# Kernel tuning notes

Hardware: AMD Instinct MI355X
Metric: run time of the kernel (lower is better)

The kernel has to match this reference:

```python
import jax, jax.numpy as jnp
from jax import lax
import numpy as np

B, C, H, W = 8, 192, 56, 56
N = H * W
K_CLUSTERS = 16   # num_centroids
K_NBRS = 9        # kNN neighbors
FACTOR = 2
COUT = C * FACTOR # hidden channels of graph conv
CPE_K = 7         # depthwise CPE kernel (odd)


def setup_inputs() -> dict:
    key = jax.random.key(0)
    ks = jax.random.split(key, 12)
    s = 0.02
    return {
        "x": jax.random.normal(ks[0], (B, C, H, W), jnp.float32),
        "labels": jax.random.randint(ks[1], (B, N), 0, K_CLUSTERS, jnp.int32),
        "cpe_w": jax.random.normal(ks[2], (C, 1, CPE_K, CPE_K), jnp.float32) * s,
        "cpe_b": jnp.zeros((C,), jnp.float32),
        "fc1_w": jax.random.normal(ks[3], (C, C), jnp.float32) * s,
        "fc1_b": jnp.zeros((C,), jnp.float32),
        "nn_v_w": jax.random.normal(ks[4], (2 * C, COUT), jnp.float32) * s,
        "nn_v_b": jnp.zeros((COUT,), jnp.float32),
        "nn_c_w": jax.random.normal(ks[5], (2 * C, COUT), jnp.float32) * s,
        "nn_c_b": jnp.zeros((COUT,), jnp.float32),
        "fc2_w": jax.random.normal(ks[6], (COUT, C), jnp.float32) * s,
        "fc2_b": jnp.zeros((C,), jnp.float32),
    }


def reference(x, labels, cpe_w, cpe_b, fc1_w, fc1_b, nn_v_w, nn_v_b,
              nn_c_w, nn_c_b, fc2_w, fc2_b):
    Bx, Cx, Hx, Wx = x.shape
    n = Hx * Wx
    shortcut = x
    # --- Conditional Position Encoding: depthwise conv + residual ---
    pe = lax.conv_general_dilated(
        x, cpe_w, (1, 1), "SAME", feature_group_count=Cx,
        dimension_numbers=("NCHW", "OIHW", "NCHW"))
    x = pe + cpe_b[None, :, None, None] + x
    # --- fc1: 1x1 conv ---
    xf = jnp.einsum("bchw,cd->bdhw", x, fc1_w) + fc1_b[None, :, None, None]
    xn = xf.reshape(Bx, Cx, n).transpose(0, 2, 1)  # [B,N,C]
    # --- organize_and_map: stable sort nodes by cluster label ---
    order = jnp.argsort(labels, axis=1)            # sorted pos -> orig idx (stable)
    mapping = jnp.argsort(order, axis=1)           # orig idx -> sorted pos
    xs = jnp.take_along_axis(xn, order[:, :, None], axis=1)  # [B,N,C]
    ls = jnp.take_along_axis(labels, order, axis=1)          # [B,N]
    # --- kNN on l2-normalized feats, restricted to same cluster ---
    xe = xs / jnp.maximum(jnp.linalg.norm(xs, axis=-1, keepdims=True), 1e-12)
    sq = jnp.sum(xe * xe, axis=-1)                 # [B,N]
    d2 = sq[:, :, None] + sq[:, None, :] - 2.0 * jnp.einsum("bnc,bmc->bnm", xe, xe)
    same = ls[:, :, None] == ls[:, None, :]        # [B,N,N] cluster mask
    d2 = jnp.where(same, d2, jnp.inf)
    _, nbr = lax.top_k(-d2, K_NBRS)                # [B,N,k] nearest in-cluster
    valid = jnp.take_along_axis(same, nbr, axis=2) # False when cluster < k
    # --- vertex edge conv: max_j MLP([x_i, x_j - x_i]) ---
    xj = jax.vmap(lambda xb, nb: xb[nb])(xs, nbr)  # [B,N,k,C]
    xi = xs[:, :, None, :]
    msg = jnp.concatenate([jnp.broadcast_to(xi, xj.shape), xj - xi], axis=-1)
    h = jax.nn.gelu(msg @ nn_v_w + nn_v_b)         # [B,N,k,COUT]
    h = jnp.where(valid[..., None], h, -jnp.inf)   # self is always valid
    hv = jnp.max(h, axis=2)                        # [B,N,COUT]
    # --- centroid edge conv over cluster centers (fully connected per image) ---
    onehot = (ls[:, :, None] == jnp.arange(K_CLUSTERS)[None, None, :]).astype(xs.dtype)
    cnt = jnp.maximum(onehot.sum(axis=1), 1.0)     # [B,K]
    cen = jnp.einsum("bnk,bnc->bkc", onehot, xs) / cnt[:, :, None]
    ci = cen[:, :, None, :]
    cj = cen[:, None, :, :]
    cmsg = jnp.concatenate(
        [jnp.broadcast_to(ci, (Bx, K_CLUSTERS, K_CLUSTERS, Cx)), cj - ci], axis=-1)
    hc = jnp.max(jax.nn.gelu(cmsg @ nn_c_w + nn_c_b), axis=2)  # [B,K,COUT]
    hcn = jax.vmap(lambda hb, lb: hb[lb])(hc, ls)  # scatter center feat to nodes
    hn = hv + hcn                                  # [B,N,COUT]
    # --- unshuffle back to original raster order ---
    out_nodes = jnp.take_along_axis(hn, mapping[:, :, None], axis=1)
    # --- fc2: 1x1 conv back to C, residual ---
    y = out_nodes @ fc2_w + fc2_b                  # [B,N,C]
    y = y.transpose(0, 2, 1).reshape(Bx, Cx, Hx, Wx)
    return y + shortcut
```

## Files before the change

kernel.cpp:

```cpp
#include <hip/hip_runtime.h>
#include <math.h>

#define NB 8
#define NC 192
#define NH 56
#define NW 56
#define NN 3136
#define NK 16
#define KNB 9
#define NCOUT 384
#define LPMAX 320
#define DSTRIDE 320
#define DSLOT (320 * 320)

#define FLT_INF __builtin_inff()

typedef short s16x8 __attribute__((ext_vector_type(8)));
typedef _Float16 f16x8 __attribute__((ext_vector_type(8)));
typedef float f32x4 __attribute__((ext_vector_type(4)));
typedef unsigned short us8 __attribute__((ext_vector_type(8)));
typedef unsigned short us4 __attribute__((ext_vector_type(4)));

__device__ __forceinline__ float gelu_t(float x) {
    const float k0 = 0.7978845608028654f;
    float u = k0 * (x + 0.044715f * x * x * x);
    float t = tanhf(u);
    return 0.5f * x * (1.0f + t);
}

__device__ __forceinline__ unsigned short f2bf(float f) {
    unsigned u = __float_as_uint(f);
    u += 0x7fff + ((u >> 16) & 1);
    return (unsigned short)(u >> 16);
}

__device__ __forceinline__ float bf2f(unsigned short h) {
    return __uint_as_float(((unsigned)h) << 16);
}

__global__ void order_kernel(const int* __restrict__ labels, int* __restrict__ order,
                             int* __restrict__ mapping, int* __restrict__ lsv,
                             int* __restrict__ cntk, int* __restrict__ offk) {
    int b = blockIdx.x >> 4;
    int k = blockIdx.x & 15;
    int lane = threadIdx.x;
    const int* lb = labels + (size_t)b * NN;
    int cntLess = 0, cntEq = 0;
    for (int n0 = 0; n0 < NN; n0 += 64) {
        int lab = lb[n0 + lane] & 15;
        cntLess += __popcll(__ballot(lab < k));
        cntEq += __popcll(__ballot(lab == k));
    }
    int base = cntLess;
    int run = 0;
    for (int n0 = 0; n0 < NN; n0 += 64) {
        int n = n0 + lane;
        int lab = lb[n] & 15;
        bool p = (lab == k);
        unsigned long long mask = __ballot(p);
        int rank = __popcll(mask & ((1ull << lane) - 1ull));
        if (p) {
            int pos = base + run + rank;
            order[b * NN + pos] = n;
            mapping[b * NN + n] = pos;
            lsv[b * NN + pos] = k;
        }
        run += __popcll(mask);
    }
    if (lane == 0) {
        offk[b * NK + k] = base;
        cntk[b * NK + k] = cntEq;
    }
}

__global__ __launch_bounds__(256) void conv_kernel(const float* __restrict__ X,
                                                   const float* __restrict__ W7,
                                                   const float* __restrict__ bias,
                                                   unsigned short* __restrict__ xpe) {
    __shared__ float tile[62 * 62];
    __shared__ float wl[49];
    int bc = blockIdx.x;
    int c = bc % NC;
    const float* Xp = X + (size_t)bc * NN;
    int tid = threadIdx.x;
    if (tid < 49) wl[tid] = W7[(size_t)c * 49 + tid];
    for (int idx = tid; idx < 62 * 62; idx += 256) {
        int ty = idx / 62, tx = idx % 62;
        int gy = ty - 3, gx = tx - 3;
        float v = 0.0f;
        if (gy >= 0 && gy < NH && gx >= 0 && gx < NW) v = Xp[gy * NW + gx];
        tile[idx] = v;
    }
    __syncthreads();
    float cb = bias[c];
    for (int g = tid; g < (NN / 4); g += 256) {
        int y = g / (NW / 4), x0 = (g % (NW / 4)) * 4;
        float a0 = 0.f, a1 = 0.f, a2 = 0.f, a3 = 0.f;
#pragma unroll
        for (int dy = 0; dy < 7; ++dy) {
            const float* tr = &tile[(y + dy) * 62 + x0];
#pragma unroll
            for (int dx = 0; dx < 7; ++dx) {
                float wv = wl[dy * 7 + dx];
                a0 += tr[dx] * wv;
                a1 += tr[dx + 1] * wv;
                a2 += tr[dx + 2] * wv;
                a3 += tr[dx + 3] * wv;
            }
        }
        const float* rr = &tile[(y + 3) * 62 + x0 + 3];
        us4 o;
        o[0] = f2bf(a0 + cb + rr[0]);
        o[1] = f2bf(a1 + cb + rr[1]);
        o[2] = f2bf(a2 + cb + rr[2]);
        o[3] = f2bf(a3 + cb + rr[3]);
        *(us4*)(xpe + (size_t)bc * NN + y * NW + x0) = o;
    }
}

__global__ void wcvt_all_kernel(const float* __restrict__ Wf1, const float* __restrict__ Wv,
                                const float* __restrict__ Wf2, unsigned short* __restrict__ wf1,
                                unsigned short* __restrict__ wfpmq,
                                unsigned short* __restrict__ wfq,
                                unsigned short* __restrict__ wf2) {
    int z = blockIdx.z, nt = blockIdx.x, kc = blockIdx.y;
    const float* W;
    unsigned short* Bf;
    int ldw, rowoff, KC, NT;
    bool diff = false;
    if (z == 0) { W = Wf1; Bf = wf1; ldw = NC; rowoff = 0; KC = 6; NT = 3; }
    else if (z == 1) { W = Wv; Bf = wfpmq; ldw = NCOUT; rowoff = 0; KC = 6; NT = 6; diff = true; }
    else if (z == 2) { W = Wv; Bf = wfq; ldw = NCOUT; rowoff = NC; KC = 6; NT = 6; }
    else { W = Wf2; Bf = wf2; ldw = NC; rowoff = 0; KC = 12; NT = 3; }
    if (nt >= NT || kc >= KC) return;
    int tid = threadIdx.x;
    int c = tid >> 6, l = tid & 63;
    int n = l & 15, q = l >> 4;
    int col = nt * 64 + c * 16 + n;
    int krow = rowoff + kc * 32 + q * 8;
    unsigned short pack[8];
#pragma unroll
    for (int j = 0; j < 8; ++j) {
        float v = W[(size_t)(krow + j) * ldw + col];
        if (diff) v -= W[(size_t)(NC + krow + j) * ldw + col];
        pack[j] = f2bf(v);
    }
    *(us8*)(Bf + ((((size_t)nt * KC + kc) * 4 + c) * 64 + l) * 8) = *(const us8*)pack;
}

__global__ __launch_bounds__(256) void tcvt_kernel(const unsigned short* __restrict__ xpe,
                                                   unsigned short* __restrict__ Af) {
    __shared__ unsigned short t[32][72];
    int b = blockIdx.z, kc = blockIdx.y, n0 = blockIdx.x * 64;
    int tid = threadIdx.x;
    int cl = tid >> 3, nl = (tid & 7) * 8;
    const unsigned short* src = xpe + ((size_t)b * NC + kc * 32 + cl) * NN + n0 + nl;
    *(us8*)&t[cl][nl] = *(const us8*)src;
    __syncthreads();
    int w = tid >> 6, l = tid & 63;
    int m = l & 15, q = l >> 4;
    int nloc = w * 16 + m;
    unsigned short pack[8];
#pragma unroll
    for (int j = 0; j < 8; ++j) pack[j] = t[q * 8 + j][nloc];
    int sg = blockIdx.x * 4 + w;
    *(us8*)(Af + (size_t)b * NN * NC + (((size_t)sg * 6 + kc) * 64 + l) * 8) =
        *(const us8*)pack;
}

template <int KC>
__global__ __launch_bounds__(256) void gemm_mfma(const unsigned short* __restrict__ Af,
                                                 size_t aStride,
                                                 const unsigned short* __restrict__ Bf,
                                                 const float* __restrict__ bias,
                                                 float* __restrict__ C, size_t cStride,
                                                 int ldc, unsigned short* __restrict__ Cfrag,
                                                 const int* __restrict__ rowmap) {
    int b = blockIdx.z;
    int w = threadIdx.x >> 6, lane = threadIdx.x & 63;
    int sg = blockIdx.y * 4 + w;
    int n0 = blockIdx.x * 64;
    const unsigned short* Ap = Af + (size_t)b * aStride + ((size_t)sg * KC * 64 + lane) * 8;
    const unsigned short* Bp = Bf + ((size_t)blockIdx.x * KC * 256 + lane) * 8;
    f32x4 acc[4] = {};
#pragma unroll
    for (int kc = 0; kc < KC; ++kc) {
        s16x8 a = *(const s16x8*)(Ap + kc * 512);
#pragma unroll
        for (int c = 0; c < 4; ++c) {
            s16x8 bv = *(const s16x8*)(Bp + kc * 2048 + c * 512);
            acc[c] = __builtin_amdgcn_mfma_f32_16x16x32_bf16(a, bv, acc[c], 0, 0, 0);
        }
    }
    int col0 = lane & 15, rq = lane >> 4;
    float* Cb = C + (size_t)b * cStride;
    int kcd = ldc >> 5;
#pragma unroll
    for (int r = 0; r < 4; ++r) {
        int grow = sg * 16 + rq * 4 + r;
        int orow = rowmap ? rowmap[(size_t)b * NN + grow] : grow;
#pragma unroll
        for (int c = 0; c < 4; ++c) {
            int col = n0 + c * 16 + col0;
            float v = acc[c][r];
            if (bias) v += bias[col];
            Cb[(size_t)orow * ldc + col] = v;
            if (Cfrag) {
                int s2 = orow >> 4, m2 = orow & 15;
                int kc2 = col >> 5, q2 = (col >> 3) & 3, j2 = col & 7;
                Cfrag[(size_t)b * cStride +
                      (((size_t)s2 * kcd + kc2) * 64 + q2 * 16 + m2) * 8 + j2] = f2bf(v);
            }
        }
    }
}

template <int KC>
__global__ __launch_bounds__(256) void gemm_mfma_pq(const unsigned short* __restrict__ Af,
                                                    size_t aStride,
                                                    const unsigned short* __restrict__ B1,
                                                    const unsigned short* __restrict__ B2,
                                                    const float* __restrict__ bias,
                                                    unsigned short* __restrict__ PmQ,
                                                    unsigned short* __restrict__ Qh,
                                                    size_t cStride, int ldc) {
    int b = blockIdx.z;
    int w = threadIdx.x >> 6, lane = threadIdx.x & 63;
    int sg = blockIdx.y * 4 + w;
    int n0 = blockIdx.x * 64;
    const unsigned short* Ap = Af + (size_t)b * aStride + ((size_t)sg * KC * 64 + lane) * 8;
    const unsigned short* Bp1 = B1 + ((size_t)blockIdx.x * KC * 256 + lane) * 8;
    const unsigned short* Bp2 = B2 + ((size_t)blockIdx.x * KC * 256 + lane) * 8;
    f32x4 acc1[4] = {};
    f32x4 acc2[4] = {};
#pragma unroll
    for (int kc = 0; kc < KC; ++kc) {
        s16x8 a = *(const s16x8*)(Ap + kc * 512);
#pragma unroll
        for (int c = 0; c < 4; ++c) {
            s16x8 b1 = *(const s16x8*)(Bp1 + kc * 2048 + c * 512);
            acc1[c] = __builtin_amdgcn_mfma_f32_16x16x32_bf16(a, b1, acc1[c], 0, 0, 0);
            s16x8 b2 = *(const s16x8*)(Bp2 + kc * 2048 + c * 512);
            acc2[c] = __builtin_amdgcn_mfma_f32_16x16x32_bf16(a, b2, acc2[c], 0, 0, 0);
        }
    }
    int col0 = lane & 15, rq = lane >> 4;
    unsigned short* Pb = PmQ + (size_t)b * cStride;
    unsigned short* Qb = Qh + (size_t)b * cStride;
#pragma unroll
    for (int r = 0; r < 4; ++r) {
        int grow = sg * 16 + rq * 4 + r;
#pragma unroll
        for (int c = 0; c < 4; ++c) {
            int col = n0 + c * 16 + col0;
            Pb[(size_t)grow * ldc + col] = f2bf(acc1[c][r] + bias[col]);
            Qb[(size_t)grow * ldc + col] = f2bf(acc2[c][r]);
        }
    }
}

template <int KC>
__global__ __launch_bounds__(256) void gemm_mfma_hb(const unsigned short* __restrict__ Af,
                                                    size_t aStride,
                                                    const unsigned short* __restrict__ Bf,
                                                    const float* __restrict__ bias,
                                                    unsigned short* __restrict__ C,
                                                    size_t cStride, int ldc,
                                                    const int* __restrict__ rowmap) {
    int b = blockIdx.z;
    int w = threadIdx.x >> 6, lane = threadIdx.x & 63;
    int sg = blockIdx.y * 4 + w;
    int n0 = blockIdx.x * 64;
    const unsigned short* Ap = Af + (size_t)b * aStride + ((size_t)sg * KC * 64 + lane) * 8;
    const unsigned short* Bp = Bf + ((size_t)blockIdx.x * KC * 256 + lane) * 8;
    f32x4 acc[4] = {};
#pragma unroll
    for (int kc = 0; kc < KC; ++kc) {
        s16x8 a = *(const s16x8*)(Ap + kc * 512);
#pragma unroll
        for (int c = 0; c < 4; ++c) {
            s16x8 bv = *(const s16x8*)(Bp + kc * 2048 + c * 512);
            acc[c] = __builtin_amdgcn_mfma_f32_16x16x32_bf16(a, bv, acc[c], 0, 0, 0);
        }
    }
    int col0 = lane & 15, rq = lane >> 4;
    unsigned short* Cb = C + (size_t)b * cStride;
#pragma unroll
    for (int r = 0; r < 4; ++r) {
        int grow = sg * 16 + rq * 4 + r;
        int orow = rowmap[(size_t)b * NN + grow];
#pragma unroll
        for (int c = 0; c < 4; ++c) {
            int col = n0 + c * 16 + col0;
            Cb[(size_t)orow * ldc + col] = f2bf(acc[c][r] + bias[col]);
        }
    }
}

__global__ __launch_bounds__(384) void xe_cvt_kernel(const float* __restrict__ xs,
                                                     const int* __restrict__ offk,
                                                     const int* __restrict__ cntk,
                                                     _Float16* __restrict__ xef,
                                                     float* __restrict__ sqv) {
    __shared__ float psum[16][25];
    __shared__ float rloc[16];
    int b = blockIdx.z, k = blockIdx.y, strip = blockIdx.x;
    int bk = b * NK + k;
    int base = offk[bk], L = cntk[bk];
    if (strip * 16 >= L) return;
    int kc = threadIdx.x >> 6, l = threadIdx.x & 63;
    int m = l & 15, q = l >> 4;
    int rl = strip * 16 + m;
    int row = base + (rl < L ? rl : L - 1);
    const float* src = xs + ((size_t)b * NN + row) * NC + kc * 32 + q * 8;
    float4 v0 = *(const float4*)src;
    float4 v1 = *(const float4*)(src + 4);
    float part = v0.x * v0.x + v0.y * v0.y + v0.z * v0.z + v0.w * v0.w + v1.x * v1.x +
                 v1.y * v1.y + v1.z * v1.z + v1.w * v1.w;
    psum[m][kc * 4 + q] = part;
    __syncthreads();
    if (threadIdx.x < 16) {
        float s = 0.0f;
#pragma unroll
        for (int i2 = 0; i2 < 24; ++i2) s += psum[threadIdx.x][i2];
        float nrm = fmaxf(sqrtf(s), 1e-12f);
        float ri = 1.0f / nrm;
        rloc[threadIdx.x] = ri;
        if (strip * 16 + (int)threadIdx.x < L)
            sqv[(size_t)b * NN + base + strip * 16 + threadIdx.x] = (s * ri) * ri;
    }
    __syncthreads();
    float rv = rloc[m];
    f16x8 pack;
    pack[0] = (_Float16)(v0.x * rv);
    pack[1] = (_Float16)(v0.y * rv);
    pack[2] = (_Float16)(v0.z * rv);
    pack[3] = (_Float16)(v0.w * rv);
    pack[4] = (_Float16)(v1.x * rv);
    pack[5] = (_Float16)(v1.y * rv);
    pack[6] = (_Float16)(v1.z * rv);
    pack[7] = (_Float16)(v1.w * rv);
    *(f16x8*)(xef + (size_t)bk * (20 * 6 * 512) + (((size_t)strip * 6 + kc) * 64 + l) * 8) =
        pack;
}

__global__ __launch_bounds__(256) void gram_kernel(const _Float16* __restrict__ xef,
                                                   const float* __restrict__ sqv,
                                                   const int* __restrict__ offk,
                                                   const int* __restrict__ cntk,
                                                   float* __restrict__ D) {
    int bk = blockIdx.z;
    int b = bk >> 4;
    int base = offk[bk], L = cntk[bk];
    int ti = blockIdx.x, tj = blockIdx.y;
    if (ti * 64 >= L || tj * 64 >= L) return;
    int w = threadIdx.x >> 6, lane = threadIdx.x & 63;
    const _Float16* Xf = xef + (size_t)bk * (20 * 6 * 512);
    const _Float16* Ap = Xf + (((size_t)(ti * 4 + w) * 6) * 64 + lane) * 8;
    f32x4 acc[4] = {};
#pragma unroll
    for (int kc = 0; kc < 6; ++kc) {
        f16x8 a = *(const f16x8*)(Ap + kc * 512);
#pragma unroll
        for (int js = 0; js < 4; ++js) {
            f16x8 bv = *(const f16x8*)(Xf + (((size_t)(tj * 4 + js) * 6 + kc) * 64 + lane) * 8);
            acc[js] = __builtin_amdgcn_mfma_f32_16x16x32_f16(a, bv, acc[js], 0, 0, 0);
        }
    }
    float* Dr = D + (size_t)bk * DSLOT;
    const float* Sb = sqv + (size_t)b * NN + base;
    int col0 = lane & 15, rq = lane >> 4;
#pragma unroll
    for (int r = 0; r < 4; ++r) {
        int i = ti * 64 + w * 16 + rq * 4 + r;
        if (i >= L) continue;
        float si = Sb[i];
#pragma unroll
        for (int js = 0; js < 4; ++js) {
            int j = tj * 64 + js * 16 + col0;
            if (j < L) Dr[(size_t)i * DSTRIDE + j] = si + Sb[j] - 2.0f * acc[js][r];
        }
    }
}

#define LEXLT(da, ca, db, cb) ((da) < (db) || ((da) == (db) && (ca) < (cb)))
__global__ __launch_bounds__(256) void select9_kernel(const float* __restrict__ D,
                                                      const int* __restrict__ lsv,
                                                      const int* __restrict__ offk,
                                                      const int* __restrict__ cntk,
                                                      int* __restrict__ nbr) {
    int b = blockIdx.y;
    int r = blockIdx.x * 4 + (threadIdx.x >> 6);
    int lane = threadIdx.x & 63;
    int k = lsv[(size_t)b * NN + r];
    int bk = b * NK + k;
    int base = offk[bk], L = cntk[bk];
    int Lc = L < LPMAX ? L : LPMAX;
    const float* Dr = D + (size_t)bk * DSLOT + (size_t)(r - base) * DSTRIDE;
    float d0, d1, d2, d3, d4;
    int c0, c1, c2, c3, c4;
    c0 = lane;
    c1 = lane + 64;
    c2 = lane + 128;
    c3 = lane + 192;
    c4 = lane + 256;
    d0 = c0 < Lc ? Dr[c0] : FLT_INF;
    d1 = c1 < Lc ? Dr[c1] : FLT_INF;
    d2 = c2 < Lc ? Dr[c2] : FLT_INF;
    d3 = c3 < Lc ? Dr[c3] : FLT_INF;
    d4 = c4 < Lc ? Dr[c4] : FLT_INF;
#define CS(da, ca, db, cb)                  \
    if (LEXLT(db, cb, da, ca)) {            \
        float t = da; da = db; db = t;      \
        int u = ca; ca = cb; cb = u;        \
    }
    CS(d0, c0, d1, c1) CS(d3, c3, d4, c4) CS(d2, c2, d4, c4) CS(d2, c2, d3, c3)
    CS(d1, c1, d4, c4) CS(d0, c0, d3, c3) CS(d0, c0, d2, c2) CS(d1, c1, d3, c3)
    CS(d1, c1, d2, c2)
#undef CS
    size_t row = (size_t)b * NN + r;
    for (int q = 0; q < KNB; ++q) {
        float bd = d0;
        int bc = c0;
#pragma unroll
        for (int m = 32; m; m >>= 1) {
            float od = __shfl_xor(bd, m, 64);
            int oc = __shfl_xor(bc, m, 64);
            if (LEXLT(od, oc, bd, bc)) {
                bd = od;
                bc = oc;
            }
        }
        if (lane == 0) nbr[row * KNB + q] = base + bc;
        if (d0 == bd && c0 == bc) {
            d0 = d1; c0 = c1;
            d1 = d2; c1 = c2;
            d2 = d3; c2 = c3;
            d3 = d4; c3 = c4;
            d4 = FLT_INF; c4 = 0x7fffffff;
        }
    }
}

__global__ __launch_bounds__(768) void cen_kernel(const float* __restrict__ xs,
                                                  const int* __restrict__ offk,
                                                  const int* __restrict__ cntk,
                                                  float* __restrict__ cen) {
    __shared__ float part[4][NC];
    int bk = blockIdx.x;
    int b = bk >> 4;
    int base = offk[bk], L = cntk[bk];
    int w = threadIdx.x / NC;
    int c = threadIdx.x % NC;
    const float* Xb = xs + ((size_t)b * NN + base) * NC + c;
    float s = 0.0f;
    for (int r = w; r < L; r += 4) s += Xb[(size_t)r * NC];
    part[w][c] = s;
    __syncthreads();
    if (threadIdx.x < NC) {
        int cc = threadIdx.x;
        float tot = part[0][cc] + part[1][cc] + part[2][cc] + part[3][cc];
        cen[(size_t)bk * NC + cc] = tot / fmaxf((float)L, 1.0f);
    }
}

__global__ __launch_bounds__(384) void pcqc_kernel(const float* __restrict__ cen,
                                                   const float* __restrict__ Wc,
                                                   const float* __restrict__ bc,
                                                   float* __restrict__ Pc,
                                                   float* __restrict__ Qc) {
    __shared__ float ce[NC];
    int bk = blockIdx.x;
    int o = threadIdx.x;
    if (o < NC) ce[o] = cen[(size_t)bk * NC + o];
    __syncthreads();
    float pc = bc[o], qc = 0.0f;
    for (int c = 0; c < NC; ++c) {
        pc += ce[c] * Wc[(size_t)c * NCOUT + o];
        qc += ce[c] * Wc[(size_t)(NC + c) * NCOUT + o];
    }
    Pc[(size_t)bk * NCOUT + o] = pc;
    Qc[(size_t)bk * NCOUT + o] = qc;
}

__global__ __launch_bounds__(384) void hcmax_kernel(const float* __restrict__ Pc,
                                                    const float* __restrict__ Qc,
                                                    float* __restrict__ hc) {
    int b = blockIdx.x >> 4, i = blockIdx.x & 15;
    int o = threadIdx.x;
    float pi = Pc[((size_t)b * NK + i) * NCOUT + o];
    float qi = Qc[((size_t)b * NK + i) * NCOUT + o];
    float pmq = pi - qi;
    float qmn = FLT_INF, qmx = -FLT_INF;
    for (int j = 0; j < NK; ++j) {
        float v = Qc[((size_t)b * NK + j) * NCOUT + o];
        qmn = fminf(qmn, v);
        qmx = fmaxf(qmx, v);
    }
    hc[((size_t)b * NK + i) * NCOUT + o] =
        fmaxf(gelu_t(pmq + qmn), gelu_t(pmq + qmx));
}

__global__ __launch_bounds__(256) void hv_kernel(const unsigned short* __restrict__ PmQ,
                                                 const unsigned short* __restrict__ Qh,
                                                 const int* __restrict__ nbr,
                                                 const int* __restrict__ lsv,
                                                 const float* __restrict__ hc,
                                                 unsigned short* __restrict__ hnf) {
    __shared__ float hnv[4][NCOUT];
    int b = blockIdx.y;
    int w = threadIdx.x >> 6, lane = threadIdx.x & 63;
    int i = blockIdx.x * 4 + w;
    size_t row = (size_t)b * NN + i;
    const unsigned short* Pr = PmQ + row * NCOUT;
    int lab = lsv[row];
    const float* hcr = hc + ((size_t)b * NK + lab) * NCOUT;
    int jn[KNB];
#pragma unroll
    for (int q = 0; q < KNB; ++q) jn[q] = nbr[row * KNB + q];
    const unsigned short* Qbb = Qh + (size_t)b * NN * NCOUT;
#pragma unroll
    for (int u = 0; u < 6; ++u) {
        int o = lane + 64 * u;
        float pmq = bf2f(Pr[o]);
        float q0 = bf2f(Qbb[(size_t)jn[0] * NCOUT + o]);
        float qmn = q0, qmx = q0;
#pragma unroll
        for (int q = 1; q < KNB; ++q) {
            float v = bf2f(Qbb[(size_t)jn[q] * NCOUT + o]);
            qmn = fminf(qmn, v);
            qmx = fmaxf(qmx, v);
        }
        float m = fmaxf(gelu_t(pmq + qmn), gelu_t(pmq + qmx));
        hnv[w][o] = m + hcr[o];
    }
    __syncthreads();
    if (threadIdx.x < 192) {
        int rsub = threadIdx.x / 48, c = threadIdx.x % 48;
        int i2 = blockIdx.x * 4 + rsub;
        int s = i2 >> 4, mm = i2 & 15;
        unsigned short pack[8];
#pragma unroll
        for (int e = 0; e < 8; ++e) pack[e] = f2bf(hnv[rsub][c * 8 + e]);
        *(us8*)(hnf + (size_t)b * NN * NCOUT +
                (((size_t)s * 12 + (c >> 2)) * 64 + (c & 3) * 16 + mm) * 8) =
            *(const us8*)pack;
    }
}

__global__ void out_kernel(const unsigned short* __restrict__ T, const float* __restrict__ X,
                           float* __restrict__ Y) {
    __shared__ float t[32][33];
    int b = blockIdx.z;
    int n0 = blockIdx.y * 32, c0 = blockIdx.x * 32;
    int tx = threadIdx.x, ty = threadIdx.y;
#pragma unroll
    for (int q = 0; q < 4; ++q) {
        int n = n0 + ty + q * 8;
        t[ty + q * 8][tx] = bf2f(T[((size_t)b * NN + n) * NC + c0 + tx]);
    }
    __syncthreads();
#pragma unroll
    for (int q = 0; q < 4; ++q) {
        int c = c0 + ty + q * 8;
        size_t idx = ((size_t)b * NC + c) * NN + n0 + tx;
        Y[idx] = t[tx][ty + q * 8] + X[idx];
    }
}

extern "C" void kernel_launch(void* const* d_in, const int* in_sizes, int n_in, void* d_out,
                              int out_size, void* d_ws, size_t ws_size, hipStream_t stream) {
    const float* x = (const float*)d_in[0];
    const int* labels = (const int*)d_in[1];
    const float* cpe_w = (const float*)d_in[2];
    const float* cpe_b = (const float*)d_in[3];
    const float* fc1_w = (const float*)d_in[4];
    const float* fc1_b = (const float*)d_in[5];
    const float* nn_v_w = (const float*)d_in[6];
    const float* nn_v_b = (const float*)d_in[7];
    const float* nn_c_w = (const float*)d_in[8];
    const float* nn_c_b = (const float*)d_in[9];
    const float* fc2_w = (const float*)d_in[10];
    const float* fc2_b = (const float*)d_in[11];
    float* out = (float*)d_out;

    const size_t SZ_XS = (size_t)NB * NN * NC;
    const size_t SZ_P = (size_t)NB * NN * NCOUT;
    const size_t BN = (size_t)NB * NN;
    const size_t SZ_CEN = (size_t)NB * NK * NC;
    const size_t SZ_PC = (size_t)NB * NK * NCOUT;

    float* base = (float*)d_ws;
    float* xs = base;
    float* xpeRegion = xs + SZ_XS;
    float* Pb = xpeRegion + SZ_XS;
    float* Qb = Pb + SZ_P;
    float* rinv = Qb + SZ_P;
    float* sqv = rinv + BN;
    float* cen = sqv + BN;
    float* Pc = cen + SZ_CEN;
    float* Qc = Pc + SZ_PC;
    float* hcv = Qc + SZ_PC;
    int* order = (int*)(hcv + SZ_PC);
    int* mapping = order + BN;
    int* lsv = mapping + BN;
    int* nbrv = lsv + BN;
    int* cntk = nbrv + BN * KNB;
    int* offk = cntk + NB * NK;
    unsigned short* xpe = (unsigned short*)xpeRegion;
    float* Dbuf = Pb;
    unsigned short* PmQh = (unsigned short*)Pb;
    unsigned short* Qh = (unsigned short*)Qb;
    unsigned short* out_t = (unsigned short*)xs;
    unsigned short* frag = (unsigned short*)(offk + NB * NK);
    unsigned short* xpeT_frag = frag;
    unsigned short* xs_frag = frag + SZ_XS;
    unsigned short* hn_frag = frag;
    unsigned short* wf1 = frag + 2 * SZ_XS;
    unsigned short* wfpmq = wf1 + (size_t)NC * NC;
    unsigned short* wfq = wfpmq + (size_t)NC * NCOUT;
    unsigned short* wf2 = wfq + (size_t)NC * NCOUT;
    _Float16* xef = (_Float16*)(wf2 + (size_t)NCOUT * NC);

    order_kernel<<<NB * NK, 64, 0, stream>>>(labels, order, mapping, lsv, cntk, offk);
    wcvt_all_kernel<<<dim3(6, 12, 4), 256, 0, stream>>>(fc1_w, nn_v_w, fc2_w, wf1, wfpmq,
                                                        wfq, wf2);
    conv_kernel<<<NB * NC, 256, 0, stream>>>(x, cpe_w, cpe_b, xpe);
    tcvt_kernel<<<dim3(NN / 64, NC / 32, NB), 256, 0, stream>>>(xpe, xpeT_frag);
    gemm_mfma<6><<<dim3(NC / 64, NN / 64, NB), 256, 0, stream>>>(
        xpeT_frag, SZ_XS / NB, wf1, fc1_b, xs, (size_t)NN * NC, NC, xs_frag, mapping);
    xe_cvt_kernel<<<dim3(LPMAX / 16, NK, NB), 384, 0, stream>>>(xs, offk, cntk, xef, sqv);
    gram_kernel<<<dim3(LPMAX / 64, LPMAX / 64, NB * NK), 256, 0, stream>>>(xef, sqv, offk,
                                                                           cntk, Dbuf);
    select9_kernel<<<dim3(NN / 4, NB), 256, 0, stream>>>(Dbuf, lsv, offk, cntk, nbrv);
    gemm_mfma_pq<6><<<dim3(NCOUT / 64, NN / 64, NB), 256, 0, stream>>>(
        xs_frag, SZ_XS / NB, wfpmq, wfq, nn_v_b, PmQh, Qh, (size_t)NN * NCOUT, NCOUT);
    cen_kernel<<<NB * NK, 768, 0, stream>>>(xs, offk, cntk, cen);
    pcqc_kernel<<<NB * NK, NCOUT, 0, stream>>>(cen, nn_c_w, nn_c_b, Pc, Qc);
    hcmax_kernel<<<NB * NK, NCOUT, 0, stream>>>(Pc, Qc, hcv);
    hv_kernel<<<dim3(NN / 4, NB), 256, 0, stream>>>(PmQh, Qh, nbrv, lsv, hcv, hn_frag);
    gemm_mfma_hb<12><<<dim3(NC / 64, NN / 64, NB), 256, 0, stream>>>(
        hn_frag, SZ_P / NB, wf2, fc2_b, out_t, (size_t)NN * NC, NC, order);
    out_kernel<<<dim3(NC / 32, NN / 32, NB), dim3(32, 8), 0, stream>>>(out_t, x, out);
}
```

Before: 317.6 us.

## Merge front kernels, fuse centroid projection, vectorize hv gather, cheaper GELU

Folds the order, weight-conversion and depthwise conv kernels into one launch, splitting work by block index. It also merges the centroid mean with the Pc/Qc projection, rewrites hv_kernel so each thread gathers 8 contiguous bf16 values per neighbour row with no shared-memory staging, and replaces tanhf in GELU with an exp and fast-reciprocal sigmoid form. The aim is fewer launches, fewer serial dependencies and less scalar memory traffic. The fast reciprocal and exp form change rounding slightly, and the merged front kernel runs order blocks with mostly idle threads.

```diff
diff --git a/kernel.cpp b/kernel.cpp
--- a/kernel.cpp
+++ b/kernel.cpp
@@ -24,8 +24,8 @@
 __device__ __forceinline__ float gelu_t(float x) {
     const float k0 = 0.7978845608028654f;
     float u = k0 * (x + 0.044715f * x * x * x);
-    float t = tanhf(u);
-    return 0.5f * x * (1.0f + t);
+    float sg = __builtin_amdgcn_rcpf(1.0f + __expf(-2.0f * u));
+    return x * sg;
 }
 
 __device__ __forceinline__ unsigned short f2bf(float f) {
@@ -38,114 +38,116 @@
     return __uint_as_float(((unsigned)h) << 16);
 }
 
-__global__ void order_kernel(const int* __restrict__ labels, int* __restrict__ order,
-                             int* __restrict__ mapping, int* __restrict__ lsv,
-                             int* __restrict__ cntk, int* __restrict__ offk) {
-    int b = blockIdx.x >> 4;
-    int k = blockIdx.x & 15;
-    int lane = threadIdx.x;
-    const int* lb = labels + (size_t)b * NN;
-    int cntLess = 0, cntEq = 0;
-    for (int n0 = 0; n0 < NN; n0 += 64) {
-        int lab = lb[n0 + lane] & 15;
-        cntLess += __popcll(__ballot(lab < k));
-        cntEq += __popcll(__ballot(lab == k));
-    }
-    int base = cntLess;
-    int run = 0;
-    for (int n0 = 0; n0 < NN; n0 += 64) {
-        int n = n0 + lane;
-        int lab = lb[n] & 15;
-        bool p = (lab == k);
-        unsigned long long mask = __ballot(p);
-        int rank = __popcll(mask & ((1ull << lane) - 1ull));
-        if (p) {
-            int pos = base + run + rank;
-            order[b * NN + pos] = n;
-            mapping[b * NN + n] = pos;
-            lsv[b * NN + pos] = k;
-        }
-        run += __popcll(mask);
-    }
-    if (lane == 0) {
-        offk[b * NK + k] = base;
-        cntk[b * NK + k] = cntEq;
-    }
-}
-
-__global__ __launch_bounds__(256) void conv_kernel(const float* __restrict__ X,
-                                                   const float* __restrict__ W7,
-                                                   const float* __restrict__ bias,
-                                                   unsigned short* __restrict__ xpe) {
+#define FRONT_CONV_BLOCKS (NB * NC)
+#define FRONT_ORDER_BLOCKS (NB * NK)
+#define FRONT_WCVT_BLOCKS 288
+__global__ __launch_bounds__(256) void front_kernel(
+    const float* __restrict__ X, const float* __restrict__ W7, const float* __restrict__ bias,
+    unsigned short* __restrict__ xpe,
+    const int* __restrict__ labels, int* __restrict__ order, int* __restrict__ mapping,
+    int* __restrict__ lsv, int* __restrict__ cntk, int* __restrict__ offk,
+    const float* __restrict__ Wf1, const float* __restrict__ Wv, const float* __restrict__ Wf2,
+    unsigned short* __restrict__ wf1, unsigned short* __restrict__ wfpmq,
+    unsigned short* __restrict__ wfq, unsigned short* __restrict__ wf2) {
     __shared__ float tile[62 * 62];
     __shared__ float wl[49];
-    int bc = blockIdx.x;
-    int c = bc % NC;
-    const float* Xp = X + (size_t)bc * NN;
+    int bid = blockIdx.x;
     int tid = threadIdx.x;
-    if (tid < 49) wl[tid] = W7[(size_t)c * 49 + tid];
-    for (int idx = tid; idx < 62 * 62; idx += 256) {
-        int ty = idx / 62, tx = idx % 62;
-        int gy = ty - 3, gx = tx - 3;
-        float v = 0.0f;
-        if (gy >= 0 && gy < NH && gx >= 0 && gx < NW) v = Xp[gy * NW + gx];
-        tile[idx] = v;
-    }
-    __syncthreads();
-    float cb = bias[c];
-    for (int g = tid; g < (NN / 4); g += 256) {
-        int y = g / (NW / 4), x0 = (g % (NW / 4)) * 4;
-        float a0 = 0.f, a1 = 0.f, a2 = 0.f, a3 = 0.f;
-#pragma unroll
-        for (int dy = 0; dy < 7; ++dy) {
-            const float* tr = &tile[(y + dy) * 62 + x0];
-#pragma unroll
-            for (int dx = 0; dx < 7; ++dx) {
-                float wv = wl[dy * 7 + dx];
-                a0 += tr[dx] * wv;
-                a1 += tr[dx + 1] * wv;
-                a2 += tr[dx + 2] * wv;
-                a3 += tr[dx + 3] * wv;
+    if (bid < FRONT_CONV_BLOCKS) {
+        int bc = bid;
+        int c = bc % NC;
+        const float* Xp = X + (size_t)bc * NN;
+        if (tid < 49) wl[tid] = W7[(size_t)c * 49 + tid];
+        for (int idx = tid; idx < 62 * 62; idx += 256) {
+            int ty = idx / 62, tx = idx % 62;
+            int gy = ty - 3, gx = tx - 3;
+            float v = 0.0f;
+            if (gy >= 0 && gy < NH && gx >= 0 && gx < NW) v = Xp[gy * NW + gx];
+            tile[idx] = v;
+        }
+        __syncthreads();
+        float cb = bias[c];
+        for (int g = tid; g < (NN / 4); g += 256) {
+            int y = g / (NW / 4), x0 = (g % (NW / 4)) * 4;
+            float a0 = 0.f, a1 = 0.f, a2 = 0.f, a3 = 0.f;
+#pragma unroll
+            for (int dy = 0; dy < 7; ++dy) {
+                const float* tr = &tile[(y + dy) * 62 + x0];
+#pragma unroll
+                for (int dx = 0; dx < 7; ++dx) {
+                    float wv = wl[dy * 7 + dx];
+                    a0 += tr[dx] * wv;
+                    a1 += tr[dx + 1] * wv;
+                    a2 += tr[dx + 2] * wv;
+                    a3 += tr[dx + 3] * wv;
+                }
             }
-        }
-        const float* rr = &tile[(y + 3) * 62 + x0 + 3];
-        us4 o;
-        o[0] = f2bf(a0 + cb + rr[0]);
-        o[1] = f2bf(a1 + cb + rr[1]);
-        o[2] = f2bf(a2 + cb + rr[2]);
-        o[3] = f2bf(a3 + cb + rr[3]);
-        *(us4*)(xpe + (size_t)bc * NN + y * NW + x0) = o;
-    }
-}
-
-__global__ void wcvt_all_kernel(const float* __restrict__ Wf1, const float* __restrict__ Wv,
-                                const float* __restrict__ Wf2, unsigned short* __restrict__ wf1,
-                                unsigned short* __restrict__ wfpmq,
-                                unsigned short* __restrict__ wfq,
-                                unsigned short* __restrict__ wf2) {
-    int z = blockIdx.z, nt = blockIdx.x, kc = blockIdx.y;
-    const float* W;
-    unsigned short* Bf;
-    int ldw, rowoff, KC, NT;
-    bool diff = false;
-    if (z == 0) { W = Wf1; Bf = wf1; ldw = NC; rowoff = 0; KC = 6; NT = 3; }
-    else if (z == 1) { W = Wv; Bf = wfpmq; ldw = NCOUT; rowoff = 0; KC = 6; NT = 6; diff = true; }
-    else if (z == 2) { W = Wv; Bf = wfq; ldw = NCOUT; rowoff = NC; KC = 6; NT = 6; }
-    else { W = Wf2; Bf = wf2; ldw = NC; rowoff = 0; KC = 12; NT = 3; }
-    if (nt >= NT || kc >= KC) return;
-    int tid = threadIdx.x;
-    int c = tid >> 6, l = tid & 63;
-    int n = l & 15, q = l >> 4;
-    int col = nt * 64 + c * 16 + n;
-    int krow = rowoff + kc * 32 + q * 8;
-    unsigned short pack[8];
-#pragma unroll
-    for (int j = 0; j < 8; ++j) {
-        float v = W[(size_t)(krow + j) * ldw + col];
-        if (diff) v -= W[(size_t)(NC + krow + j) * ldw + col];
-        pack[j] = f2bf(v);
-    }
-    *(us8*)(Bf + ((((size_t)nt * KC + kc) * 4 + c) * 64 + l) * 8) = *(const us8*)pack;
+            const float* rr = &tile[(y + 3) * 62 + x0 + 3];
+            us4 o;
+            o[0] = f2bf(a0 + cb + rr[0]);
+            o[1] = f2bf(a1 + cb + rr[1]);
+            o[2] = f2bf(a2 + cb + rr[2]);
+            o[3] = f2bf(a3 + cb + rr[3]);
+            *(us4*)(xpe + (size_t)bc * NN + y * NW + x0) = o;
+        }
+    } else if (bid < FRONT_CONV_BLOCKS + FRONT_ORDER_BLOCKS) {
+        if (tid >= 64) return;
+        int idx = bid - FRONT_CONV_BLOCKS;
+        int b = idx >> 4;
+        int k = idx & 15;
+        int lane = tid;
+        const int* lb = labels + (size_t)b * NN;
+        int cntLess = 0, cntEq = 0;
+        for (int n0 = 0; n0 < NN; n0 += 64) {
+            int lab = lb[n0 + lane] & 15;
+            cntLess += __popcll(__ballot(lab < k));
+            cntEq += __popcll(__ballot(lab == k));
+        }
+        int base = cntLess;
+        int run = 0;
+        for (int n0 = 0; n0 < NN; n0 += 64) {
+            int n = n0 + lane;
+            int lab = lb[n] & 15;
+            bool p = (lab == k);
+            unsigned long long mask = __ballot(p);
+            int rank = __popcll(mask & ((1ull << lane) - 1ull));
+            if (p) {
+                int pos = base + run + rank;
+                order[b * NN + pos] = n;
+                mapping[b * NN + n] = pos;
+                lsv[b * NN + pos] = k;
+            }
+            run += __popcll(mask);
+        }
+        if (lane == 0) {
+            offk[b * NK + k] = base;
+            cntk[b * NK + k] = cntEq;
+        }
+    } else {
+        int u = bid - (FRONT_CONV_BLOCKS + FRONT_ORDER_BLOCKS);
+        int nt = u % 6, kc = (u / 6) % 12, z = u / 72;
+        const float* W;
+        unsigned short* Bf;
+        int ldw, rowoff, KC, NT;
+        bool diff = false;
+        if (z == 0) { W = Wf1; Bf = wf1; ldw = NC; rowoff = 0; KC = 6; NT = 3; }
+        else if (z == 1) { W = Wv; Bf = wfpmq; ldw = NCOUT; rowoff = 0; KC = 6; NT = 6; diff = true; }
+        else if (z == 2) { W = Wv; Bf = wfq; ldw = NCOUT; rowoff = NC; KC = 6; NT = 6; }
+        else { W = Wf2; Bf = wf2; ldw = NC; rowoff = 0; KC = 12; NT = 3; }
+        if (nt >= NT || kc >= KC) return;
+        int c = tid >> 6, l = tid & 63;
+        int n = l & 15, q = l >> 4;
+        int col = nt * 64 + c * 16 + n;
+        int krow = rowoff + kc * 32 + q * 8;
+        unsigned short pack[8];
+#pragma unroll
+        for (int j = 0; j < 8; ++j) {
+            float v = W[(size_t)(krow + j) * ldw + col];
+            if (diff) v -= W[(size_t)(NC + krow + j) * ldw + col];
+            pack[j] = f2bf(v);
+        }
+        *(us8*)(Bf + ((((size_t)nt * KC + kc) * 4 + c) * 64 + l) * 8) = *(const us8*)pack;
+    }
 }
 
 __global__ __launch_bounds__(256) void tcvt_kernel(const unsigned short* __restrict__ xpe,
@@ -442,11 +444,16 @@
     }
 }
 
-__global__ __launch_bounds__(768) void cen_kernel(const float* __restrict__ xs,
-                                                  const int* __restrict__ offk,
-                                                  const int* __restrict__ cntk,
-                                                  float* __restrict__ cen) {
+__global__ __launch_bounds__(768) void cenpq_kernel(const float* __restrict__ xs,
+                                                    const int* __restrict__ offk,
+                                                    const int* __restrict__ cntk,
+                                                    const float* __restrict__ Wc,
+                                                    const float* __restrict__ bc,
+                                                    float* __restrict__ Pc,
+                                                    float* __restrict__ Qc) {
     __shared__ float part[4][NC];
+    __shared__ float ce[NC];
+    __shared__ float pcs[NCOUT], qcs[NCOUT];
     int bk = blockIdx.x;
     int b = bk >> 4;
     int base = offk[bk], L = cntk[bk];
@@ -460,27 +467,26 @@
     if (threadIdx.x < NC) {
         int cc = threadIdx.x;
         float tot = part[0][cc] + part[1][cc] + part[2][cc] + part[3][cc];
-        cen[(size_t)bk * NC + cc] = tot / fmaxf((float)L, 1.0f);
-    }
-}
-
-__global__ __launch_bounds__(384) void pcqc_kernel(const float* __restrict__ cen,
-                                                   const float* __restrict__ Wc,
-                                                   const float* __restrict__ bc,
-                                                   float* __restrict__ Pc,
-                                                   float* __restrict__ Qc) {
-    __shared__ float ce[NC];
-    int bk = blockIdx.x;
-    int o = threadIdx.x;
-    if (o < NC) ce[o] = cen[(size_t)bk * NC + o];
+        ce[cc] = tot / fmaxf((float)L, 1.0f);
+    }
     __syncthreads();
-    float pc = bc[o], qc = 0.0f;
-    for (int c = 0; c < NC; ++c) {
-        pc += ce[c] * Wc[(size_t)c * NCOUT + o];
-        qc += ce[c] * Wc[(size_t)(NC + c) * NCOUT + o];
-    }
-    Pc[(size_t)bk * NCOUT + o] = pc;
-    Qc[(size_t)bk * NCOUT + o] = qc;
+    int o = threadIdx.x % NCOUT, half = threadIdx.x / NCOUT;
+    float pc = 0.0f, qc = 0.0f;
+    int cs = half * 96, cend = cs + 96;
+    for (int c2 = cs; c2 < cend; ++c2) {
+        float cv = ce[c2];
+        pc += cv * Wc[(size_t)c2 * NCOUT + o];
+        qc += cv * Wc[(size_t)(NC + c2) * NCOUT + o];
+    }
+    if (half == 1) {
+        pcs[o] = pc;
+        qcs[o] = qc;
+    }
+    __syncthreads();
+    if (half == 0) {
+        Pc[(size_t)bk * NCOUT + o] = pc + pcs[o] + bc[o];
+        Qc[(size_t)bk * NCOUT + o] = qc + qcs[o];
+    }
 }
 
 __global__ __launch_bounds__(384) void hcmax_kernel(const float* __restrict__ Pc,
@@ -501,51 +507,56 @@
         fmaxf(gelu_t(pmq + qmn), gelu_t(pmq + qmx));
 }
 
-__global__ __launch_bounds__(256) void hv_kernel(const unsigned short* __restrict__ PmQ,
+__global__ __launch_bounds__(192) void hv_kernel(const unsigned short* __restrict__ PmQ,
                                                  const unsigned short* __restrict__ Qh,
                                                  const int* __restrict__ nbr,
                                                  const int* __restrict__ lsv,
                                                  const float* __restrict__ hc,
                                                  unsigned short* __restrict__ hnf) {
-    __shared__ float hnv[4][NCOUT];
     int b = blockIdx.y;
-    int w = threadIdx.x >> 6, lane = threadIdx.x & 63;
-    int i = blockIdx.x * 4 + w;
+    int t = threadIdx.x;
+    int rsub = t / 48, c = t % 48;
+    int i = blockIdx.x * 4 + rsub;
     size_t row = (size_t)b * NN + i;
-    const unsigned short* Pr = PmQ + row * NCOUT;
     int lab = lsv[row];
-    const float* hcr = hc + ((size_t)b * NK + lab) * NCOUT;
+    int o0 = c * 8;
     int jn[KNB];
 #pragma unroll
     for (int q = 0; q < KNB; ++q) jn[q] = nbr[row * KNB + q];
-    const unsigned short* Qbb = Qh + (size_t)b * NN * NCOUT;
-#pragma unroll
-    for (int u = 0; u < 6; ++u) {
-        int o = lane + 64 * u;
-        float pmq = bf2f(Pr[o]);
-        float q0 = bf2f(Qbb[(size_t)jn[0] * NCOUT + o]);
-        float qmn = q0, qmx = q0;
-#pragma unroll
-        for (int q = 1; q < KNB; ++q) {
-            float v = bf2f(Qbb[(size_t)jn[q] * NCOUT + o]);
-            qmn = fminf(qmn, v);
-            qmx = fmaxf(qmx, v);
-        }
-        float m = fmaxf(gelu_t(pmq + qmn), gelu_t(pmq + qmx));
-        hnv[w][o] = m + hcr[o];
-    }
-    __syncthreads();
-    if (threadIdx.x < 192) {
-        int rsub = threadIdx.x / 48, c = threadIdx.x % 48;
-        int i2 = blockIdx.x * 4 + rsub;
-        int s = i2 >> 4, mm = i2 & 15;
-        unsigned short pack[8];
-#pragma unroll
-        for (int e = 0; e < 8; ++e) pack[e] = f2bf(hnv[rsub][c * 8 + e]);
-        *(us8*)(hnf + (size_t)b * NN * NCOUT +
-                (((size_t)s * 12 + (c >> 2)) * 64 + (c & 3) * 16 + mm) * 8) =
-            *(const us8*)pack;
-    }
+    const unsigned short* Qbb = Qh + (size_t)b * NN * NCOUT + o0;
+    us8 pv = *(const us8*)(PmQ + row * NCOUT + o0);
+    us8 q0 = *(const us8*)(Qbb + (size_t)jn[0] * NCOUT);
+    float qmn[8], qmx[8];
+#pragma unroll
+    for (int e = 0; e < 8; ++e) {
+        float v = bf2f(q0[e]);
+        qmn[e] = v;
+        qmx[e] = v;
+    }
+#pragma unroll
+    for (int q = 1; q < KNB; ++q) {
+        us8 qv = *(const us8*)(Qbb + (size_t)jn[q] * NCOUT);
+#pragma unroll
+        for (int e = 0; e < 8; ++e) {
+            float v = bf2f(qv[e]);
+            qmn[e] = fminf(qmn[e], v);
+            qmx[e] = fmaxf(qmx[e], v);
+        }
+    }
+    const float* hcr = hc + ((size_t)b * NK + lab) * NCOUT + o0;
+    float4 h0 = *(const float4*)hcr;
+    float4 h1 = *(const float4*)(hcr + 4);
+    float hcv[8] = {h0.x, h0.y, h0.z, h0.w, h1.x, h1.y, h1.z, h1.w};
+    unsigned short pack[8];
+#pragma unroll
+    for (int e = 0; e < 8; ++e) {
+        float pmq = bf2f(pv[e]);
+        float m = fmaxf(gelu_t(pmq + qmn[e]), gelu_t(pmq + qmx[e]));
+        pack[e] = f2bf(m + hcv[e]);
+    }
+    int s = i >> 4, mm = i & 15;
+    *(us8*)(hnf + (size_t)b * NN * NCOUT +
+            (((size_t)s * 12 + (c >> 2)) * 64 + (c & 3) * 16 + mm) * 8) = *(const us8*)pack;
 }
 
 __global__ void out_kernel(const unsigned short* __restrict__ T, const float* __restrict__ X,
@@ -622,10 +633,9 @@
     unsigned short* wf2 = wfq + (size_t)NC * NCOUT;
     _Float16* xef = (_Float16*)(wf2 + (size_t)NCOUT * NC);
 
-    order_kernel<<<NB * NK, 64, 0, stream>>>(labels, order, mapping, lsv, cntk, offk);
-    wcvt_all_kernel<<<dim3(6, 12, 4), 256, 0, stream>>>(fc1_w, nn_v_w, fc2_w, wf1, wfpmq,
-                                                        wfq, wf2);
-    conv_kernel<<<NB * NC, 256, 0, stream>>>(x, cpe_w, cpe_b, xpe);
+    front_kernel<<<FRONT_CONV_BLOCKS + FRONT_ORDER_BLOCKS + FRONT_WCVT_BLOCKS, 256, 0, stream>>>(
+        x, cpe_w, cpe_b, xpe, labels, order, mapping, lsv, cntk, offk, fc1_w, nn_v_w, fc2_w,
+        wf1, wfpmq, wfq, wf2);
     tcvt_kernel<<<dim3(NN / 64, NC / 32, NB), 256, 0, stream>>>(xpe, xpeT_frag);
     gemm_mfma<6><<<dim3(NC / 64, NN / 64, NB), 256, 0, stream>>>(
         xpeT_frag, SZ_XS / NB, wf1, fc1_b, xs, (size_t)NN * NC, NC, xs_frag, mapping);
@@ -635,10 +645,9 @@
     select9_kernel<<<dim3(NN / 4, NB), 256, 0, stream>>>(Dbuf, lsv, offk, cntk, nbrv);
     gemm_mfma_pq<6><<<dim3(NCOUT / 64, NN / 64, NB), 256, 0, stream>>>(
         xs_frag, SZ_XS / NB, wfpmq, wfq, nn_v_b, PmQh, Qh, (size_t)NN * NCOUT, NCOUT);
-    cen_kernel<<<NB * NK, 768, 0, stream>>>(xs, offk, cntk, cen);
-    pcqc_kernel<<<NB * NK, NCOUT, 0, stream>>>(cen, nn_c_w, nn_c_b, Pc, Qc);
+    cenpq_kernel<<<NB * NK, 768, 0, stream>>>(xs, offk, cntk, nn_c_w, nn_c_b, Pc, Qc);
     hcmax_kernel<<<NB * NK, NCOUT, 0, stream>>>(Pc, Qc, hcv);
-    hv_kernel<<<dim3(NN / 4, NB), 256, 0, stream>>>(PmQh, Qh, nbrv, lsv, hcv, hn_frag);
+    hv_kernel<<<dim3(NN / 4, NB), 192, 0, stream>>>(PmQh, Qh, nbrv, lsv, hcv, hn_frag);
     gemm_mfma_hb<12><<<dim3(NC / 64, NN / 64, NB), 256, 0, stream>>>(
         hn_frag, SZ_P / NB, wf2, fc2_b, out_t, (size_t)NN * NC, NC, order);
     out_kernel<<<dim3(NC / 32, NN / 32, NB), dim3(32, 8), 0, stream>>>(out_t, x, out);
```

Result: faster. 297.1 us (-6.5%).
